# Performance work log

Measured on AMD Instinct MI355X. Metric: run time of the kernel, lower is better.

## Reference

```python
import jax, jax.numpy as jnp
import numpy as np

NF = 64            # nf_effect
N_HISTORY = 3
ADJ_THRESH = 0.12  # float adj_thresh passed to construct_edges
PSTEP = 3


def _relu(x):
    return jnp.maximum(x, 0)


def construct_edges(states, thresh, mask, tool_mask, topk):
    """JAX port of construct_edges_from_states_batch (connect_tools_all=False).
    Returns fixed-shape Rr, Rs of shape (B, N*topk, N); each receiver i owns
    slots [i*topk, (i+1)*topk). Invalid slots are all-zero rows, which is
    math-equivalent to torch's compacted n_rel under all bmms.
    """
    B, N, _ = states.shape
    dt = states.dtype
    d = states[:, :, None, :] - states[:, None, :, :]          # (B,N,N,3)
    dis = jnp.sum(d * d, axis=-1)                              # (B,N,N)
    big = jnp.asarray(1e10, dt)
    m12 = mask[:, :, None] & mask[:, None, :]                  # valid pair
    t12 = tool_mask[:, :, None] & tool_mask[:, None, :]        # tool-tool: cut
    dis = jnp.where(m12 & ~t12, dis, big)
    adj = dis < (thresh * thresh)                              # (B,N,N) bool
    # connect_tools_all=False branch: zero tool-receiver / obj-sender edges
    adj = adj & ~(tool_mask[:, :, None] & mask[:, None, :])
    _, idx = jax.lax.top_k(-dis, topk)                         # (B,N,topk) smallest dis
    valid = jnp.take_along_axis(adj, idx, axis=-1).astype(dt)  # (B,N,topk)
    recv_oh = jnp.eye(N, dtype=dt)                             # (N,N)
    Rr = (valid[..., None] * recv_oh[None, :, None, :]).reshape(B, N * topk, N)
    Rs = (valid[..., None] * jax.nn.one_hot(idx, N, dtype=dt)).reshape(B, N * topk, N)
    return Rr, Rs


def _prop_forward(states, a_cur, s_delta, Rr, Rs,
                  pe_w1, pe_b1, pe_w2, pe_b2,
                  re_w1, re_b1, re_w2, re_b2, re_w3, re_b3,
                  rp_w, rp_b, pp_w, pp_b,
                  pr_w1, pr_b1, pr_w2, pr_b2):
    # s_delta: (B, 3*n_history, N) -> (B, N, 3*n_history)
    s_delta_flat = jnp.transpose(s_delta, (0, 2, 1))
    nh = N_HISTORY
    # relation features: receiver/sender attrs + position difference
    a_r = jnp.einsum('brn,bn->br', Rr, a_cur)[..., None]       # (B,R,1)
    a_s = jnp.einsum('brn,bn->br', Rs, a_cur)[..., None]
    s_r = jnp.einsum('brn,bnd->brd', Rr, states)               # (B,R,3)
    s_s = jnp.einsum('brn,bnd->brd', Rs, states)
    rel_in = jnp.concatenate([a_r, a_s, s_r - s_s], axis=-1)   # (B,R,5)
    # relation encoder: 3-layer MLP, ReLU after each
    h = _relu(rel_in @ re_w1 + re_b1)
    h = _relu(h @ re_w2 + re_b2)
    rel_enc = _relu(h @ re_w3 + re_b3)                         # (B,R,NF)
    # particle encoder: [s_delta history | attrs tiled n_history] -> 12 dims
    p_in = jnp.concatenate(
        [s_delta_flat, jnp.repeat(a_cur[..., None], nh, axis=-1)], axis=-1)
    p_enc = _relu(_relu(p_in @ pe_w1 + pe_b1) @ pe_w2 + pe_b2)  # (B,N,NF)
    effect = p_enc
    for _ in range(PSTEP):
        eff_r = jnp.einsum('brn,bnd->brd', Rr, effect)
        eff_s = jnp.einsum('brn,bnd->brd', Rs, effect)
        rel_eff = _relu(
            jnp.concatenate([rel_enc, eff_r, eff_s], axis=-1) @ rp_w + rp_b)
        agg = jnp.einsum('brn,brd->bnd', Rr, rel_eff)          # Rr^T bmm
        effect = _relu(
            jnp.concatenate([p_enc, agg], axis=-1) @ pp_w + pp_b + effect)
    pred = _relu(effect @ pr_w1 + pr_b1) @ pr_w2 + pr_b2       # (B,N,3)
    return states + pred  # add_delta=True


def setup_inputs():
    key = jax.random.key(0)
    ks = jax.random.split(key, 16)
    B, N = 2, 2048
    states = jax.random.uniform(ks[0], (B, N, 3), dtype=jnp.float32)
    a_cur = jax.random.uniform(ks[1], (B, N), dtype=jnp.float32)
    s_delta = jax.random.normal(ks[2], (B, 3 * N_HISTORY, N), dtype=jnp.float32) * 0.01
    mask = jnp.ones((B, N), dtype=bool)
    tool_mask = jnp.broadcast_to(jnp.arange(N) < N // 20, (B, N))
    s = lambda fan: 1.0 / np.sqrt(fan)
    p = lambda k, sh: jax.random.normal(k, sh, dtype=jnp.float32) * s(sh[0])
    z = lambda n: jnp.zeros((n,), dtype=jnp.float32)
    params = {
        'pe_w1': p(ks[3], (4 * N_HISTORY, NF)), 'pe_b1': z(NF),
        'pe_w2': p(ks[4], (NF, NF)), 'pe_b2': z(NF),
        're_w1': p(ks[5], (5, NF)), 're_b1': z(NF),
        're_w2': p(ks[6], (NF, NF)), 're_b2': z(NF),
        're_w3': p(ks[7], (NF, NF)), 're_b3': z(NF),
        'rp_w': p(ks[8], (3 * NF, NF)), 'rp_b': z(NF),
        'pp_w': p(ks[9], (2 * NF, NF)), 'pp_b': z(NF),
        'pr_w1': p(ks[10], (NF, NF)), 'pr_b1': z(NF),
        'pr_w2': p(ks[11], (NF, 3)), 'pr_b2': z(3),
    }
    return {'states': states, 'a_cur': a_cur, 's_delta': s_delta,
            'mask': mask, 'tool_mask': tool_mask, 'topk': 8, **params}


def reference(states, a_cur, s_delta, mask, tool_mask, topk,
              pe_w1, pe_b1, pe_w2, pe_b2,
              re_w1, re_b1, re_w2, re_b2, re_w3, re_b3,
              rp_w, rp_b, pp_w, pp_b,
              pr_w1, pr_b1, pr_w2, pr_b2):
    Rr, Rs = construct_edges(states, ADJ_THRESH, mask, tool_mask, topk)
    return _prop_forward(states, a_cur, s_delta, Rr, Rs,
                         pe_w1, pe_b1, pe_w2, pe_b2,
                         re_w1, re_b1, re_w2, re_b2, re_w3, re_b3,
                         rp_w, rp_b, pp_w, pp_b,
                         pr_w1, pr_b1, pr_w2, pr_b2)
```

## Files before the change

### kernel.cpp

```cpp
#include <hip/hip_runtime.h>
#include <math.h>

#define DEV __device__ __forceinline__

constexpr int BB = 2, N = 2048, KK = 8;
constexpr int NODES = BB * N;
constexpr int NSLOTS = NODES * KK;
constexpr int NPB = 8;
constexpr int TPB = 512;
constexpr int NBLK = NODES / NPB;

typedef __attribute__((ext_vector_type(8))) short short8v;
typedef __attribute__((ext_vector_type(4))) float float4v;
union S8 { short8v v; unsigned u[4]; unsigned short s[8]; };

DEV int bool_mode(const void* p) {
  unsigned v = *(const unsigned*)p;
  if (v == 0x3f800000u) return 2;
  if (v <= 1u) return 1;
  return 0;
}
DEV bool read_mask(const void* p, int i, int mode) {
  if (mode == 2) return ((const float*)p)[i] != 0.f;
  if (mode == 1) return ((const int*)p)[i] != 0;
  return ((const unsigned char*)p)[i] != 0;
}

DEV unsigned short f2bf(float x) {
  unsigned u = __builtin_bit_cast(unsigned, x);
  return (unsigned short)((u + 0x7FFFu + ((u >> 16) & 1u)) >> 16);
}
DEV unsigned pk2(float a, float b) {
  return (unsigned)f2bf(a) | ((unsigned)f2bf(b) << 16);
}

DEV short8v rdA(const unsigned short* T, int row, int kk0) {
  return *(const short8v*)&T[row * 64 + (kk0 ^ ((row & 7) << 3))];
}
DEV void stage_wT(const float* __restrict__ W, unsigned short* wt, int t) {
  const int f = t & 63, k0 = (t >> 6) * 8;
  S8 p;
  #pragma unroll
  for (int q = 0; q < 4; ++q)
    p.u[q] = pk2(W[(k0 + 2 * q) * 64 + f], W[(k0 + 2 * q + 1) * 64 + f]);
  *(short8v*)&wt[f * 64 + (k0 ^ ((f & 7) << 3))] = p.v;
}
DEV void stage_row8(unsigned short* T, int row, int kq, const float* __restrict__ g) {
  const int k0 = kq * 8;
  float4 v0 = ((const float4*)(g + k0))[0];
  float4 v1 = ((const float4*)(g + k0))[1];
  S8 p;
  p.u[0] = pk2(v0.x, v0.y); p.u[1] = pk2(v0.z, v0.w);
  p.u[2] = pk2(v1.x, v1.y); p.u[3] = pk2(v1.z, v1.w);
  *(short8v*)&T[row * 64 + (k0 ^ ((row & 7) << 3))] = p.v;
}

#define LESS(da, ja, db, jb) ((da) < (db) || ((da) == (db) && (ja) < (jb)))
#define CE(a, b)                                                              \
  {                                                                           \
    bool sw_ = LESS(nd[b], nj[b], nd[a], nj[a]);                              \
    float t_ = nd[a]; int u_ = nj[a];                                         \
    if (sw_) { nd[a] = nd[b]; nj[a] = nj[b]; nd[b] = t_; nj[b] = u_; }        \
  }

struct SEdge { float px[N], py[N], pz[N], padd[N]; };
struct SMlpF { unsigned short A0[4096]; unsigned short A1[4096]; float hb[64 * 9]; };
union SUF { SEdge e; SMlpF m; };

__global__ __launch_bounds__(TPB, 4) void k_front(
    const float* __restrict__ states, const void* maskp, const void* toolp,
    const float* __restrict__ a_cur, const float* __restrict__ s_delta,
    const float* __restrict__ pe_w1, const float* __restrict__ pe_b1,
    const float* __restrict__ pe_w2, const float* __restrict__ pe_b2,
    const float* __restrict__ re_w1, const float* __restrict__ re_b1,
    const float* __restrict__ re_w2, const float* __restrict__ re_b2,
    const float* __restrict__ re_w3, const float* __restrict__ re_b3,
    const float* __restrict__ rp_w, const float* __restrict__ rp_b,
    const float* __restrict__ pp_w, const float* __restrict__ pp_b,
    int* __restrict__ eidx, float* __restrict__ evalid,
    float* __restrict__ p_const, float* __restrict__ rel_const,
    float* __restrict__ eff0) {
  __shared__ SUF su;
  __shared__ unsigned short wt3[3][4096];
  __shared__ int   sl_idx[64];
  __shared__ float sl_val[64];
  const int tid = threadIdx.x;
  const int wav = tid >> 6, lane = tid & 63;
  const int blk = blockIdx.x;
  const int node0 = blk * NPB;
  const int slot0 = blk * 64;
  const int b = node0 >> 11;
  const int mm = bool_mode(maskp), mt = bool_mode(toolp);

  stage_wT(re_w2, wt3[0], tid);
  stage_wT(re_w3, wt3[1], tid);
  stage_wT(rp_w,  wt3[2], tid);

  {
    for (int j = tid; j < N; j += TPB) {
      const float* s = states + (size_t)(b * N + j) * 3;
      su.e.px[j] = s[0]; su.e.py[j] = s[1]; su.e.pz[j] = s[2];
      su.e.padd[j] = read_mask(maskp, b * N + j, mm) ? 0.f : 1e10f;
    }
    __syncthreads();
    const int node = node0 + wav;
    const int i = node & (N - 1);
    const bool mi = read_mask(maskp, node, mm);
    const bool ti = read_mask(toolp, node, mt);
    float td[KK]; int tj[KK];
    #pragma unroll
    for (int k = 0; k < KK; ++k) { td[k] = 3.0e38f; tj[k] = 0; }
    if (mi && !ti) {
      const float sx = su.e.px[i], sy = su.e.py[i], sz = su.e.pz[i];
      #pragma unroll 4
      for (int it = 0; it < N / 64; ++it) {
        int j = lane + it * 64;
        float dx = sx - su.e.px[j], dy = sy - su.e.py[j], dz = sz - su.e.pz[j];
        float dis = __fadd_rn(__fadd_rn(__fmul_rn(dx, dx), __fmul_rn(dy, dy)),
                              __fmul_rn(dz, dz));
        float dd = __fadd_rn(dis, su.e.padd[j]);
        if (dd < td[KK - 1]) {
          float cd = dd; int cj = j;
          #pragma unroll
          for (int m = 0; m < KK; ++m) {
            bool sw = cd < td[m];
            float od = td[m]; int oj = tj[m];
            td[m] = sw ? cd : od; tj[m] = sw ? cj : oj;
            cd = sw ? od : cd;   cj = sw ? oj : cj;
          }
        }
      }
      #pragma unroll
      for (int m = 1; m < 64; m <<= 1) {
        float pd[KK]; int pj[KK];
        #pragma unroll
        for (int r = 0; r < KK; ++r) {
          pd[r] = __shfl_xor(td[r], m);
          pj[r] = __shfl_xor(tj[r], m);
        }
        float nd[KK]; int nj[KK];
        #pragma unroll
        for (int r = 0; r < KK; ++r) {
          float ad = td[r]; int aj = tj[r];
          float bd = pd[KK - 1 - r]; int bj = pj[KK - 1 - r];
          bool tb = LESS(bd, bj, ad, aj);
          nd[r] = tb ? bd : ad; nj[r] = tb ? bj : aj;
        }
        CE(0, 4) CE(1, 5) CE(2, 6) CE(3, 7)
        CE(0, 2) CE(1, 3) CE(4, 6) CE(5, 7)
        CE(0, 1) CE(2, 3) CE(4, 5) CE(6, 7)
        #pragma unroll
        for (int r = 0; r < KK; ++r) { td[r] = nd[r]; tj[r] = nj[r]; }
      }
    }
    if (lane == 0) {
      const float T2 = (float)(0.12 * 0.12);
      const bool ok = mi && !ti;
      #pragma unroll
      for (int k = 0; k < KK; ++k) {
        float v = (ok && td[k] < T2) ? 1.f : 0.f;
        sl_idx[wav * KK + k] = tj[k];
        sl_val[wav * KK + k] = v;
        eidx[(node0 + wav) * KK + k] = tj[k];
        evalid[(node0 + wav) * KK + k] = v;
      }
    }
    __syncthreads();
  }

  {
    float* hb = su.m.hb;
    const int nd = node0 + wav;
    const int i = nd & (N - 1);
    const int f = lane;
    float sd[9];
    #pragma unroll
    for (int k = 0; k < 9; ++k) sd[k] = s_delta[(b * 9 + k) * N + i];
    const float a = a_cur[nd];
    float x = pe_b1[f];
    #pragma unroll
    for (int k = 0; k < 9; ++k) x = fmaf(sd[k], pe_w1[k * 64 + f], x);
    x = fmaf(a, pe_w1[576 + f] + pe_w1[640 + f] + pe_w1[704 + f], x);
    x = fmaxf(x, 0.f);
    hb[f * 9 + wav] = x;
    __syncthreads();
    float y = pe_b2[f];
    #pragma unroll 4
    for (int k = 0; k < 64; ++k) y = fmaf(hb[k * 9 + wav], pe_w2[k * 64 + f], y);
    y = fmaxf(y, 0.f);
    eff0[(size_t)nd * 64 + f] = y;
    __syncthreads();
    hb[f * 9 + wav] = y;
    __syncthreads();
    float z = pp_b[f];
    #pragma unroll 4
    for (int k = 0; k < 64; ++k) z = fmaf(hb[k * 9 + wav], pp_w[k * 64 + f], z);
    p_const[(size_t)nd * 64 + f] = z;
    __syncthreads();
  }

  {
    unsigned short* A0 = su.m.A0;
    unsigned short* A1 = su.m.A1;
    const int f0 = __builtin_amdgcn_readfirstlane(wav * 8);
    const int col = lane;
    const int nd = node0 + (col >> 3);
    const int nb = nd & ~(N - 1);
    const int j = nb + sl_idx[col];
    const float a_r = a_cur[nd], a_s = a_cur[j];
    const float dx = states[nd * 3]     - states[j * 3];
    const float dy = states[nd * 3 + 1] - states[j * 3 + 1];
    const float dz = states[nd * 3 + 2] - states[j * 3 + 2];
    float t[8];
    #pragma unroll
    for (int u = 0; u < 8; ++u) {
      const int f = f0 + u;
      float x = re_b1[f];
      x = fmaf(a_r, re_w1[f], x);
      x = fmaf(a_s, re_w1[64 + f], x);
      x = fmaf(dx, re_w1[128 + f], x);
      x = fmaf(dy, re_w1[192 + f], x);
      x = fmaf(dz, re_w1[256 + f], x);
      t[u] = fmaxf(x, 0.f);
    }
    #pragma unroll
    for (int u = 0; u < 8; u += 2) {
      int idx = col * 64 + ((f0 + u) ^ ((col & 7) << 3));
      *(unsigned*)&A0[idx] = pk2(t[u], t[u + 1]);
    }
    __syncthreads();

    const int m = wav & 3, h = wav >> 2;
    const int n0t = 2 * h, n1t = n0t + 1;
    const int rowA = m * 16 + (lane & 15);
    const int fc0 = n0t * 16 + (lane & 15), fc1 = n1t * 16 + (lane & 15);
    const unsigned long long vm = __ballot(sl_val[lane] != 0.f);

    {
      float b0 = re_b2[fc0], b1 = re_b2[fc1];
      float4v c0 = {b0, b0, b0, b0}, c1 = {b1, b1, b1, b1};
      #pragma unroll
      for (int ks = 0; ks < 2; ++ks) {
        const int kk0 = ks * 32 + (lane >> 4) * 8;
        short8v a  = rdA(A0, rowA, kk0);
        short8v w0 = rdA(wt3[0], fc0, kk0);
        short8v w1 = rdA(wt3[0], fc1, kk0);
        c0 = __builtin_amdgcn_mfma_f32_16x16x32_bf16(a, w0, c0, 0, 0, 0);
        c1 = __builtin_amdgcn_mfma_f32_16x16x32_bf16(a, w1, c1, 0, 0, 0);
      }
      #pragma unroll
      for (int r = 0; r < 4; ++r) {
        int slot = m * 16 + (lane >> 4) * 4 + r;
        A1[slot * 64 + (fc0 ^ ((slot & 7) << 3))] = f2bf(fmaxf(c0[r], 0.f));
        A1[slot * 64 + (fc1 ^ ((slot & 7) << 3))] = f2bf(fmaxf(c1[r], 0.f));
      }
    }
    __syncthreads();
    {
      float b0 = re_b3[fc0], b1 = re_b3[fc1];
      float4v c0 = {b0, b0, b0, b0}, c1 = {b1, b1, b1, b1};
      #pragma unroll
      for (int ks = 0; ks < 2; ++ks) {
        const int kk0 = ks * 32 + (lane >> 4) * 8;
        short8v a  = rdA(A1, rowA, kk0);
        short8v w0 = rdA(wt3[1], fc0, kk0);
        short8v w1 = rdA(wt3[1], fc1, kk0);
        c0 = __builtin_amdgcn_mfma_f32_16x16x32_bf16(a, w0, c0, 0, 0, 0);
        c1 = __builtin_amdgcn_mfma_f32_16x16x32_bf16(a, w1, c1, 0, 0, 0);
      }
      #pragma unroll
      for (int r = 0; r < 4; ++r) {
        int slot = m * 16 + (lane >> 4) * 4 + r;
        A0[slot * 64 + (fc0 ^ ((slot & 7) << 3))] = f2bf(fmaxf(c0[r], 0.f));
        A0[slot * 64 + (fc1 ^ ((slot & 7) << 3))] = f2bf(fmaxf(c1[r], 0.f));
      }
    }
    __syncthreads();
    {
      float b0 = rp_b[fc0], b1 = rp_b[fc1];
      float4v c0 = {b0, b0, b0, b0}, c1 = {b1, b1, b1, b1};
      #pragma unroll
      for (int ks = 0; ks < 2; ++ks) {
        const int kk0 = ks * 32 + (lane >> 4) * 8;
        short8v a  = rdA(A0, rowA, kk0);
        short8v w0 = rdA(wt3[2], fc0, kk0);
        short8v w1 = rdA(wt3[2], fc1, kk0);
        c0 = __builtin_amdgcn_mfma_f32_16x16x32_bf16(a, w0, c0, 0, 0, 0);
        c1 = __builtin_amdgcn_mfma_f32_16x16x32_bf16(a, w1, c1, 0, 0, 0);
      }
      #pragma unroll
      for (int r = 0; r < 4; ++r) {
        int slot = m * 16 + (lane >> 4) * 4 + r;
        float v = (float)((vm >> slot) & 1ull);
        rel_const[(size_t)(slot0 + slot) * 64 + fc0] = c0[r] * v;
        rel_const[(size_t)(slot0 + slot) * 64 + fc1] = c1[r] * v;
      }
    }
  }
}

template <int HEAD>
__global__ __launch_bounds__(TPB, 4) void k_prop(
    const float* __restrict__ rp_w, const float* __restrict__ pp_w,
    const int* __restrict__ eidx, const float* __restrict__ evalid,
    const float* __restrict__ p_const, const float* __restrict__ rel_const,
    const float* __restrict__ effIn, float* __restrict__ effOut,
    const float* __restrict__ states,
    const float* __restrict__ pr_w1, const float* __restrict__ pr_b1,
    const float* __restrict__ pr_w2, const float* __restrict__ pr_b2,
    float* __restrict__ out) {
  __shared__ unsigned short AS[4096];
  __shared__ unsigned short EN[512];
  __shared__ unsigned short wt2[2][4096];
  __shared__ float agg[8 * 64];
  const int tid = threadIdx.x;
  const int wav = tid >> 6, lane = tid & 63;
  const int blk = blockIdx.x;
  const int node0 = blk * NPB;
  const int slot0 = blk * 64;
  const int nb = node0 & ~(N - 1);

  stage_wT(rp_w + 4096, wt2[0], tid);
  stage_wT(rp_w + 8192, wt2[1], tid);
  {
    const int slot = tid >> 3, kq = tid & 7;
    const int j = nb + eidx[slot0 + slot];
    stage_row8(AS, slot, kq, effIn + (size_t)j * 64);
  }
  if (tid < 64) {
    const int n = tid >> 3, kq = tid & 7;
    stage_row8(EN, n, kq, effIn + (size_t)(node0 + n) * 64);
  }
  const unsigned long long vm = __ballot(evalid[slot0 + lane] != 0.f);
  __syncthreads();

  {
    const int m = wav & 3, h = wav >> 2;
    const int n0t = 2 * h, n1t = n0t + 1;
    const int rowA = m * 16 + (lane & 15);
    const int nodeR = rowA >> 3;
    const int fc0 = n0t * 16 + (lane & 15), fc1 = n1t * 16 + (lane & 15);
    float4v c0, c1;
    #pragma unroll
    for (int r = 0; r < 4; ++r) {
      int slot = m * 16 + (lane >> 4) * 4 + r;
      c0[r] = rel_const[(size_t)(slot0 + slot) * 64 + fc0];
      c1[r] = rel_const[(size_t)(slot0 + slot) * 64 + fc1];
    }
    #pragma unroll
    for (int ks = 0; ks < 2; ++ks) {
      const int kk0 = ks * 32 + (lane >> 4) * 8;
      short8v aR = rdA(EN, nodeR, kk0);
      short8v aS = rdA(AS, rowA, kk0);
      short8v w10 = rdA(wt2[0], fc0, kk0);
      short8v w11 = rdA(wt2[0], fc1, kk0);
      short8v w20 = rdA(wt2[1], fc0, kk0);
      short8v w21 = rdA(wt2[1], fc1, kk0);
      c0 = __builtin_amdgcn_mfma_f32_16x16x32_bf16(aR, w10, c0, 0, 0, 0);
      c1 = __builtin_amdgcn_mfma_f32_16x16x32_bf16(aR, w11, c1, 0, 0, 0);
      c0 = __builtin_amdgcn_mfma_f32_16x16x32_bf16(aS, w20, c0, 0, 0, 0);
      c1 = __builtin_amdgcn_mfma_f32_16x16x32_bf16(aS, w21, c1, 0, 0, 0);
    }
    float s0 = 0.f, s1 = 0.f;
    #pragma unroll
    for (int r = 0; r < 4; ++r) {
      int slot = m * 16 + (lane >> 4) * 4 + r;
      float v = (float)((vm >> slot) & 1ull);
      s0 += fmaxf(c0[r], 0.f) * v;
      s1 += fmaxf(c1[r], 0.f) * v;
    }
    s0 += __shfl_xor(s0, 16);
    s1 += __shfl_xor(s1, 16);
    if (((lane >> 4) & 1) == 0) {
      const int an = m * 2 + (lane >> 5);
      agg[an * 64 + fc0] = s0;
      agg[an * 64 + fc1] = s1;
    }
  }
  __syncthreads();

  const int onode = node0 + wav;
  float o = p_const[(size_t)onode * 64 + lane];
  #pragma unroll 4
  for (int g = 0; g < 64; ++g)
    o = fmaf(agg[wav * 64 + g], pp_w[4096 + g * 64 + lane], o);
  const float er = effIn[(size_t)onode * 64 + lane];
  const float ov = fmaxf(o + er, 0.f);
  if (HEAD == 0) {
    effOut[(size_t)onode * 64 + lane] = ov;
  } else {
    __syncthreads();
    agg[wav * 64 + lane] = ov;
    __syncthreads();
    float hh = pr_b1[lane];
    #pragma unroll 4
    for (int k = 0; k < 64; ++k)
      hh = fmaf(agg[wav * 64 + k], pr_w1[k * 64 + lane], hh);
    hh = fmaxf(hh, 0.f);
    float p0 = hh * pr_w2[lane * 3];
    float p1 = hh * pr_w2[lane * 3 + 1];
    float p2 = hh * pr_w2[lane * 3 + 2];
    #pragma unroll
    for (int m = 1; m < 64; m <<= 1) {
      p0 += __shfl_xor(p0, m);
      p1 += __shfl_xor(p1, m);
      p2 += __shfl_xor(p2, m);
    }
    if (lane == 0) {
      out[onode * 3]     = states[onode * 3]     + p0 + pr_b2[0];
      out[onode * 3 + 1] = states[onode * 3 + 1] + p1 + pr_b2[1];
      out[onode * 3 + 2] = states[onode * 3 + 2] + p2 + pr_b2[2];
    }
  }
}

extern "C" void kernel_launch(void* const* d_in, const int* in_sizes, int n_in,
                              void* d_out, int out_size, void* d_ws, size_t ws_size,
                              hipStream_t stream) {
  const float* states  = (const float*)d_in[0];
  const float* a_cur   = (const float*)d_in[1];
  const float* s_delta = (const float*)d_in[2];
  const void*  maskp   = d_in[3];
  const void*  toolp   = d_in[4];
  const float* pe_w1 = (const float*)d_in[6];
  const float* pe_b1 = (const float*)d_in[7];
  const float* pe_w2 = (const float*)d_in[8];
  const float* pe_b2 = (const float*)d_in[9];
  const float* re_w1 = (const float*)d_in[10];
  const float* re_b1 = (const float*)d_in[11];
  const float* re_w2 = (const float*)d_in[12];
  const float* re_b2 = (const float*)d_in[13];
  const float* re_w3 = (const float*)d_in[14];
  const float* re_b3 = (const float*)d_in[15];
  const float* rp_w  = (const float*)d_in[16];
  const float* rp_b  = (const float*)d_in[17];
  const float* pp_w  = (const float*)d_in[18];
  const float* pp_b  = (const float*)d_in[19];
  const float* pr_w1 = (const float*)d_in[20];
  const float* pr_b1 = (const float*)d_in[21];
  const float* pr_w2 = (const float*)d_in[22];
  const float* pr_b2 = (const float*)d_in[23];

  char* w = (char*)d_ws;
  int*   eidx      = (int*)w;   w += (size_t)NSLOTS * 4;
  float* evalid    = (float*)w; w += (size_t)NSLOTS * 4;
  float* p_const   = (float*)w; w += (size_t)NODES * 64 * 4;
  float* rel_const = (float*)w; w += (size_t)NSLOTS * 64 * 4;
  float* effA      = (float*)w; w += (size_t)NODES * 64 * 4;
  float* effB      = (float*)w; w += (size_t)NODES * 64 * 4;
  float* out       = (float*)d_out;

  k_front<<<NBLK, TPB, 0, stream>>>(states, maskp, toolp, a_cur, s_delta,
      pe_w1, pe_b1, pe_w2, pe_b2, re_w1, re_b1, re_w2, re_b2, re_w3, re_b3,
      rp_w, rp_b, pp_w, pp_b, eidx, evalid, p_const, rel_const, effA);
  k_prop<0><<<NBLK, TPB, 0, stream>>>(rp_w, pp_w, eidx, evalid, p_const,
      rel_const, effA, effB, states, pr_w1, pr_b1, pr_w2, pr_b2, out);
  k_prop<0><<<NBLK, TPB, 0, stream>>>(rp_w, pp_w, eidx, evalid, p_const,
      rel_const, effB, effA, states, pr_w1, pr_b1, pr_w2, pr_b2, out);
  k_prop<1><<<NBLK, TPB, 0, stream>>>(rp_w, pp_w, eidx, evalid, p_const,
      rel_const, effA, effB, states, pr_w1, pr_b1, pr_w2, pr_b2, out);
}
```

Baseline: 161.8 us.

## Fuse front and propagation kernels into one persistent kernel with grid barriers

Merges the edge-construction/encoder kernel and the three propagation kernels into a single launch, with software grid barriers (atomic counter plus spin) between propagation steps. Per-block state such as edge indices, validity, p_const, relation constants and the node's own effect is kept in registers and LDS instead of going through global memory. This removes three kernel launches and the related global traffic. In exchange it depends on all 512 blocks being co-resident, which needs 2 blocks per CU on 256 CUs, adds a memset and spin-wait overhead, and raises LDS use per block.

```diff
diff --git a/kernel.cpp b/kernel.cpp
--- a/kernel.cpp
+++ b/kernel.cpp
@@ -5,7 +5,6 @@
 
 constexpr int BB = 2, N = 2048, KK = 8;
 constexpr int NODES = BB * N;
-constexpr int NSLOTS = NODES * KK;
 constexpr int NPB = 8;
 constexpr int TPB = 512;
 constexpr int NBLK = NODES / NPB;
@@ -64,10 +63,21 @@
   }
 
 struct SEdge { float px[N], py[N], pz[N], padd[N]; };
-struct SMlpF { unsigned short A0[4096]; unsigned short A1[4096]; float hb[64 * 9]; };
-union SUF { SEdge e; SMlpF m; };
-
-__global__ __launch_bounds__(TPB, 4) void k_front(
+
+DEV void gbar(unsigned* bar, int idx) {
+  __syncthreads();
+  if (threadIdx.x == 0) {
+    __threadfence();
+    __hip_atomic_fetch_add(&bar[idx], 1u, __ATOMIC_RELEASE, __HIP_MEMORY_SCOPE_AGENT);
+    while (__hip_atomic_load(&bar[idx], __ATOMIC_ACQUIRE,
+                             __HIP_MEMORY_SCOPE_AGENT) < (unsigned)NBLK)
+      __builtin_amdgcn_s_sleep(2);
+    __threadfence();
+  }
+  __syncthreads();
+}
+
+__global__ __launch_bounds__(TPB, 4) void k_all(
     const float* __restrict__ states, const void* maskp, const void* toolp,
     const float* __restrict__ a_cur, const float* __restrict__ s_delta,
     const float* __restrict__ pe_w1, const float* __restrict__ pe_b1,
@@ -77,30 +87,32 @@
     const float* __restrict__ re_w3, const float* __restrict__ re_b3,
     const float* __restrict__ rp_w, const float* __restrict__ rp_b,
     const float* __restrict__ pp_w, const float* __restrict__ pp_b,
-    int* __restrict__ eidx, float* __restrict__ evalid,
-    float* __restrict__ p_const, float* __restrict__ rel_const,
-    float* __restrict__ eff0) {
-  __shared__ SUF su;
-  __shared__ unsigned short wt3[3][4096];
+    const float* __restrict__ pr_w1, const float* __restrict__ pr_b1,
+    const float* __restrict__ pr_w2, const float* __restrict__ pr_b2,
+    float* __restrict__ effA, float* __restrict__ effB,
+    unsigned* __restrict__ bar, float* __restrict__ out) {
+  __shared__ unsigned short wt_rp0[4096], wt_rp1[4096], wt_rp2[4096];
+  __shared__ char Ubuf[32768];
   __shared__ int   sl_idx[64];
   __shared__ float sl_val[64];
   const int tid = threadIdx.x;
   const int wav = tid >> 6, lane = tid & 63;
   const int blk = blockIdx.x;
   const int node0 = blk * NPB;
-  const int slot0 = blk * 64;
   const int b = node0 >> 11;
+  const int nb = node0 & ~(N - 1);
   const int mm = bool_mode(maskp), mt = bool_mode(toolp);
 
-  stage_wT(re_w2, wt3[0], tid);
-  stage_wT(re_w3, wt3[1], tid);
-  stage_wT(rp_w,  wt3[2], tid);
+  stage_wT(rp_w,        wt_rp0, tid);
+  stage_wT(rp_w + 4096, wt_rp1, tid);
+  stage_wT(rp_w + 8192, wt_rp2, tid);
 
   {
+    SEdge* se = (SEdge*)Ubuf;
     for (int j = tid; j < N; j += TPB) {
       const float* s = states + (size_t)(b * N + j) * 3;
-      su.e.px[j] = s[0]; su.e.py[j] = s[1]; su.e.pz[j] = s[2];
-      su.e.padd[j] = read_mask(maskp, b * N + j, mm) ? 0.f : 1e10f;
+      se->px[j] = s[0]; se->py[j] = s[1]; se->pz[j] = s[2];
+      se->padd[j] = read_mask(maskp, b * N + j, mm) ? 0.f : 1e10f;
     }
     __syncthreads();
     const int node = node0 + wav;
@@ -111,14 +123,14 @@
     #pragma unroll
     for (int k = 0; k < KK; ++k) { td[k] = 3.0e38f; tj[k] = 0; }
     if (mi && !ti) {
-      const float sx = su.e.px[i], sy = su.e.py[i], sz = su.e.pz[i];
+      const float sx = se->px[i], sy = se->py[i], sz = se->pz[i];
       #pragma unroll 4
       for (int it = 0; it < N / 64; ++it) {
         int j = lane + it * 64;
-        float dx = sx - su.e.px[j], dy = sy - su.e.py[j], dz = sz - su.e.pz[j];
+        float dx = sx - se->px[j], dy = sy - se->py[j], dz = sz - se->pz[j];
         float dis = __fadd_rn(__fadd_rn(__fmul_rn(dx, dx), __fmul_rn(dy, dy)),
                               __fmul_rn(dz, dz));
-        float dd = __fadd_rn(dis, su.e.padd[j]);
+        float dd = __fadd_rn(dis, se->padd[j]);
         if (dd < td[KK - 1]) {
           float cd = dd; int cj = j;
           #pragma unroll
@@ -158,18 +170,20 @@
       const bool ok = mi && !ti;
       #pragma unroll
       for (int k = 0; k < KK; ++k) {
-        float v = (ok && td[k] < T2) ? 1.f : 0.f;
         sl_idx[wav * KK + k] = tj[k];
-        sl_val[wav * KK + k] = v;
-        eidx[(node0 + wav) * KK + k] = tj[k];
-        evalid[(node0 + wav) * KK + k] = v;
-      }
-    }
-    __syncthreads();
-  }
-
+        sl_val[wav * KK + k] = (ok && td[k] < T2) ? 1.f : 0.f;
+      }
+    }
+    __syncthreads();
+  }
+
+  float pc, ev;
   {
-    float* hb = su.m.hb;
+    unsigned short* wt_enc0 = (unsigned short*)(Ubuf + 16384);
+    unsigned short* wt_enc1 = (unsigned short*)(Ubuf + 24576);
+    stage_wT(re_w2, wt_enc0, tid);
+    stage_wT(re_w3, wt_enc1, tid);
+    float* hb = (float*)Ubuf;
     const int nd = node0 + wav;
     const int i = nd & (N - 1);
     const int f = lane;
@@ -188,24 +202,27 @@
     #pragma unroll 4
     for (int k = 0; k < 64; ++k) y = fmaf(hb[k * 9 + wav], pe_w2[k * 64 + f], y);
     y = fmaxf(y, 0.f);
-    eff0[(size_t)nd * 64 + f] = y;
+    effA[(size_t)nd * 64 + f] = y;
+    ev = y;
     __syncthreads();
     hb[f * 9 + wav] = y;
     __syncthreads();
     float z = pp_b[f];
     #pragma unroll 4
     for (int k = 0; k < 64; ++k) z = fmaf(hb[k * 9 + wav], pp_w[k * 64 + f], z);
-    p_const[(size_t)nd * 64 + f] = z;
+    pc = z;
     __syncthreads();
   }
 
   {
-    unsigned short* A0 = su.m.A0;
-    unsigned short* A1 = su.m.A1;
+    unsigned short* A0 = (unsigned short*)Ubuf;
+    unsigned short* A1 = (unsigned short*)(Ubuf + 8192);
+    unsigned short* wt_enc0 = (unsigned short*)(Ubuf + 16384);
+    unsigned short* wt_enc1 = (unsigned short*)(Ubuf + 24576);
+    float* relC = (float*)(Ubuf + 16384);
     const int f0 = __builtin_amdgcn_readfirstlane(wav * 8);
     const int col = lane;
     const int nd = node0 + (col >> 3);
-    const int nb = nd & ~(N - 1);
     const int j = nb + sl_idx[col];
     const float a_r = a_cur[nd], a_s = a_cur[j];
     const float dx = states[nd * 3]     - states[j * 3];
@@ -229,13 +246,10 @@
       *(unsigned*)&A0[idx] = pk2(t[u], t[u + 1]);
     }
     __syncthreads();
-
     const int m = wav & 3, h = wav >> 2;
-    const int n0t = 2 * h, n1t = n0t + 1;
     const int rowA = m * 16 + (lane & 15);
-    const int fc0 = n0t * 16 + (lane & 15), fc1 = n1t * 16 + (lane & 15);
+    const int fc0 = (2 * h) * 16 + (lane & 15), fc1 = fc0 + 16;
     const unsigned long long vm = __ballot(sl_val[lane] != 0.f);
-
     {
       float b0 = re_b2[fc0], b1 = re_b2[fc1];
       float4v c0 = {b0, b0, b0, b0}, c1 = {b1, b1, b1, b1};
@@ -243,8 +257,8 @@
       for (int ks = 0; ks < 2; ++ks) {
         const int kk0 = ks * 32 + (lane >> 4) * 8;
         short8v a  = rdA(A0, rowA, kk0);
-        short8v w0 = rdA(wt3[0], fc0, kk0);
-        short8v w1 = rdA(wt3[0], fc1, kk0);
+        short8v w0 = rdA(wt_enc0, fc0, kk0);
+        short8v w1 = rdA(wt_enc0, fc1, kk0);
         c0 = __builtin_amdgcn_mfma_f32_16x16x32_bf16(a, w0, c0, 0, 0, 0);
         c1 = __builtin_amdgcn_mfma_f32_16x16x32_bf16(a, w1, c1, 0, 0, 0);
       }
@@ -263,8 +277,8 @@
       for (int ks = 0; ks < 2; ++ks) {
         const int kk0 = ks * 32 + (lane >> 4) * 8;
         short8v a  = rdA(A1, rowA, kk0);
-        short8v w0 = rdA(wt3[1], fc0, kk0);
-        short8v w1 = rdA(wt3[1], fc1, kk0);
+        short8v w0 = rdA(wt_enc1, fc0, kk0);
+        short8v w1 = rdA(wt_enc1, fc1, kk0);
         c0 = __builtin_amdgcn_mfma_f32_16x16x32_bf16(a, w0, c0, 0, 0, 0);
         c1 = __builtin_amdgcn_mfma_f32_16x16x32_bf16(a, w1, c1, 0, 0, 0);
       }
@@ -283,8 +297,8 @@
       for (int ks = 0; ks < 2; ++ks) {
         const int kk0 = ks * 32 + (lane >> 4) * 8;
         short8v a  = rdA(A0, rowA, kk0);
-        short8v w0 = rdA(wt3[2], fc0, kk0);
-        short8v w1 = rdA(wt3[2], fc1, kk0);
+        short8v w0 = rdA(wt_rp0, fc0, kk0);
+        short8v w1 = rdA(wt_rp0, fc1, kk0);
         c0 = __builtin_amdgcn_mfma_f32_16x16x32_bf16(a, w0, c0, 0, 0, 0);
         c1 = __builtin_amdgcn_mfma_f32_16x16x32_bf16(a, w1, c1, 0, 0, 0);
       }
@@ -292,105 +306,89 @@
       for (int r = 0; r < 4; ++r) {
         int slot = m * 16 + (lane >> 4) * 4 + r;
         float v = (float)((vm >> slot) & 1ull);
-        rel_const[(size_t)(slot0 + slot) * 64 + fc0] = c0[r] * v;
-        rel_const[(size_t)(slot0 + slot) * 64 + fc1] = c1[r] * v;
-      }
-    }
-  }
-}
-
-template <int HEAD>
-__global__ __launch_bounds__(TPB, 4) void k_prop(
-    const float* __restrict__ rp_w, const float* __restrict__ pp_w,
-    const int* __restrict__ eidx, const float* __restrict__ evalid,
-    const float* __restrict__ p_const, const float* __restrict__ rel_const,
-    const float* __restrict__ effIn, float* __restrict__ effOut,
-    const float* __restrict__ states,
-    const float* __restrict__ pr_w1, const float* __restrict__ pr_b1,
-    const float* __restrict__ pr_w2, const float* __restrict__ pr_b2,
-    float* __restrict__ out) {
-  __shared__ unsigned short AS[4096];
-  __shared__ unsigned short EN[512];
-  __shared__ unsigned short wt2[2][4096];
-  __shared__ float agg[8 * 64];
-  const int tid = threadIdx.x;
-  const int wav = tid >> 6, lane = tid & 63;
-  const int blk = blockIdx.x;
-  const int node0 = blk * NPB;
-  const int slot0 = blk * 64;
-  const int nb = node0 & ~(N - 1);
-
-  stage_wT(rp_w + 4096, wt2[0], tid);
-  stage_wT(rp_w + 8192, wt2[1], tid);
+        relC[slot * 64 + fc0] = c0[r] * v;
+        relC[slot * 64 + fc1] = c1[r] * v;
+      }
+    }
+  }
+
+  gbar(bar, 0);
+
+  auto prop = [&](const float* __restrict__ effIn, float* __restrict__ effOut) {
+    unsigned short* AS = (unsigned short*)Ubuf;
+    unsigned short* EN = (unsigned short*)(Ubuf + 8192);
+    float* agg = (float*)(Ubuf + 9216);
+    float* relC = (float*)(Ubuf + 16384);
+    {
+      const int slot = tid >> 3, kq = tid & 7;
+      const int j = nb + sl_idx[slot];
+      stage_row8(AS, slot, kq, effIn + (size_t)j * 64);
+    }
+    EN[wav * 64 + (lane ^ ((wav & 7) << 3))] = f2bf(ev);
+    const unsigned long long vm = __ballot(sl_val[lane] != 0.f);
+    __syncthreads();
+    {
+      const int m = wav & 3, h = wav >> 2;
+      const int rowA = m * 16 + (lane & 15);
+      const int nodeR = rowA >> 3;
+      const int fc0 = (2 * h) * 16 + (lane & 15), fc1 = fc0 + 16;
+      float4v c0, c1;
+      #pragma unroll
+      for (int r = 0; r < 4; ++r) {
+        int slot = m * 16 + (lane >> 4) * 4 + r;
+        c0[r] = relC[slot * 64 + fc0];
+        c1[r] = relC[slot * 64 + fc1];
+      }
+      #pragma unroll
+      for (int ks = 0; ks < 2; ++ks) {
+        const int kk0 = ks * 32 + (lane >> 4) * 8;
+        short8v aR = rdA(EN, nodeR, kk0);
+        short8v aS = rdA(AS, rowA, kk0);
+        short8v w10 = rdA(wt_rp1, fc0, kk0);
+        short8v w11 = rdA(wt_rp1, fc1, kk0);
+        short8v w20 = rdA(wt_rp2, fc0, kk0);
+        short8v w21 = rdA(wt_rp2, fc1, kk0);
+        c0 = __builtin_amdgcn_mfma_f32_16x16x32_bf16(aR, w10, c0, 0, 0, 0);
+        c1 = __builtin_amdgcn_mfma_f32_16x16x32_bf16(aR, w11, c1, 0, 0, 0);
+        c0 = __builtin_amdgcn_mfma_f32_16x16x32_bf16(aS, w20, c0, 0, 0, 0);
+        c1 = __builtin_amdgcn_mfma_f32_16x16x32_bf16(aS, w21, c1, 0, 0, 0);
+      }
+      float s0 = 0.f, s1 = 0.f;
+      #pragma unroll
+      for (int r = 0; r < 4; ++r) {
+        int slot = m * 16 + (lane >> 4) * 4 + r;
+        float v = (float)((vm >> slot) & 1ull);
+        s0 += fmaxf(c0[r], 0.f) * v;
+        s1 += fmaxf(c1[r], 0.f) * v;
+      }
+      s0 += __shfl_xor(s0, 16);
+      s1 += __shfl_xor(s1, 16);
+      if (((lane >> 4) & 1) == 0) {
+        const int an = m * 2 + (lane >> 5);
+        agg[an * 64 + fc0] = s0;
+        agg[an * 64 + fc1] = s1;
+      }
+    }
+    __syncthreads();
+    float o = pc;
+    #pragma unroll 4
+    for (int g = 0; g < 64; ++g)
+      o = fmaf(agg[wav * 64 + g], pp_w[4096 + g * 64 + lane], o);
+    float ov = fmaxf(o + ev, 0.f);
+    if (effOut) effOut[(size_t)(node0 + wav) * 64 + lane] = ov;
+    ev = ov;
+    __syncthreads();
+  };
+
+  prop(effA, effB);
+  gbar(bar, 1);
+  prop(effB, effA);
+  gbar(bar, 2);
+  prop(effA, nullptr);
+
   {
-    const int slot = tid >> 3, kq = tid & 7;
-    const int j = nb + eidx[slot0 + slot];
-    stage_row8(AS, slot, kq, effIn + (size_t)j * 64);
-  }
-  if (tid < 64) {
-    const int n = tid >> 3, kq = tid & 7;
-    stage_row8(EN, n, kq, effIn + (size_t)(node0 + n) * 64);
-  }
-  const unsigned long long vm = __ballot(evalid[slot0 + lane] != 0.f);
-  __syncthreads();
-
-  {
-    const int m = wav & 3, h = wav >> 2;
-    const int n0t = 2 * h, n1t = n0t + 1;
-    const int rowA = m * 16 + (lane & 15);
-    const int nodeR = rowA >> 3;
-    const int fc0 = n0t * 16 + (lane & 15), fc1 = n1t * 16 + (lane & 15);
-    float4v c0, c1;
-    #pragma unroll
-    for (int r = 0; r < 4; ++r) {
-      int slot = m * 16 + (lane >> 4) * 4 + r;
-      c0[r] = rel_const[(size_t)(slot0 + slot) * 64 + fc0];
-      c1[r] = rel_const[(size_t)(slot0 + slot) * 64 + fc1];
-    }
-    #pragma unroll
-    for (int ks = 0; ks < 2; ++ks) {
-      const int kk0 = ks * 32 + (lane >> 4) * 8;
-      short8v aR = rdA(EN, nodeR, kk0);
-      short8v aS = rdA(AS, rowA, kk0);
-      short8v w10 = rdA(wt2[0], fc0, kk0);
-      short8v w11 = rdA(wt2[0], fc1, kk0);
-      short8v w20 = rdA(wt2[1], fc0, kk0);
-      short8v w21 = rdA(wt2[1], fc1, kk0);
-      c0 = __builtin_amdgcn_mfma_f32_16x16x32_bf16(aR, w10, c0, 0, 0, 0);
-      c1 = __builtin_amdgcn_mfma_f32_16x16x32_bf16(aR, w11, c1, 0, 0, 0);
-      c0 = __builtin_amdgcn_mfma_f32_16x16x32_bf16(aS, w20, c0, 0, 0, 0);
-      c1 = __builtin_amdgcn_mfma_f32_16x16x32_bf16(aS, w21, c1, 0, 0, 0);
-    }
-    float s0 = 0.f, s1 = 0.f;
-    #pragma unroll
-    for (int r = 0; r < 4; ++r) {
-      int slot = m * 16 + (lane >> 4) * 4 + r;
-      float v = (float)((vm >> slot) & 1ull);
-      s0 += fmaxf(c0[r], 0.f) * v;
-      s1 += fmaxf(c1[r], 0.f) * v;
-    }
-    s0 += __shfl_xor(s0, 16);
-    s1 += __shfl_xor(s1, 16);
-    if (((lane >> 4) & 1) == 0) {
-      const int an = m * 2 + (lane >> 5);
-      agg[an * 64 + fc0] = s0;
-      agg[an * 64 + fc1] = s1;
-    }
-  }
-  __syncthreads();
-
-  const int onode = node0 + wav;
-  float o = p_const[(size_t)onode * 64 + lane];
-  #pragma unroll 4
-  for (int g = 0; g < 64; ++g)
-    o = fmaf(agg[wav * 64 + g], pp_w[4096 + g * 64 + lane], o);
-  const float er = effIn[(size_t)onode * 64 + lane];
-  const float ov = fmaxf(o + er, 0.f);
-  if (HEAD == 0) {
-    effOut[(size_t)onode * 64 + lane] = ov;
-  } else {
-    __syncthreads();
-    agg[wav * 64 + lane] = ov;
+    float* agg = (float*)(Ubuf + 9216);
+    agg[wav * 64 + lane] = ev;
     __syncthreads();
     float hh = pr_b1[lane];
     #pragma unroll 4
@@ -407,6 +405,7 @@
       p2 += __shfl_xor(p2, m);
     }
     if (lane == 0) {
+      const int onode = node0 + wav;
       out[onode * 3]     = states[onode * 3]     + p0 + pr_b2[0];
       out[onode * 3 + 1] = states[onode * 3 + 1] + p1 + pr_b2[1];
       out[onode * 3 + 2] = states[onode * 3 + 2] + p2 + pr_b2[2];
@@ -442,21 +441,13 @@
   const float* pr_b2 = (const float*)d_in[23];
 
   char* w = (char*)d_ws;
-  int*   eidx      = (int*)w;   w += (size_t)NSLOTS * 4;
-  float* evalid    = (float*)w; w += (size_t)NSLOTS * 4;
-  float* p_const   = (float*)w; w += (size_t)NODES * 64 * 4;
-  float* rel_const = (float*)w; w += (size_t)NSLOTS * 64 * 4;
-  float* effA      = (float*)w; w += (size_t)NODES * 64 * 4;
-  float* effB      = (float*)w; w += (size_t)NODES * 64 * 4;
-  float* out       = (float*)d_out;
-
-  k_front<<<NBLK, TPB, 0, stream>>>(states, maskp, toolp, a_cur, s_delta,
+  float* effA = (float*)w; w += (size_t)NODES * 64 * 4;
+  float* effB = (float*)w; w += (size_t)NODES * 64 * 4;
+  unsigned* bar = (unsigned*)w;
+
+  hipMemsetAsync(bar, 0, 4 * sizeof(unsigned), stream);
+  k_all<<<NBLK, TPB, 0, stream>>>(states, maskp, toolp, a_cur, s_delta,
       pe_w1, pe_b1, pe_w2, pe_b2, re_w1, re_b1, re_w2, re_b2, re_w3, re_b3,
-      rp_w, rp_b, pp_w, pp_b, eidx, evalid, p_const, rel_const, effA);
-  k_prop<0><<<NBLK, TPB, 0, stream>>>(rp_w, pp_w, eidx, evalid, p_const,
-      rel_const, effA, effB, states, pr_w1, pr_b1, pr_w2, pr_b2, out);
-  k_prop<0><<<NBLK, TPB, 0, stream>>>(rp_w, pp_w, eidx, evalid, p_const,
-      rel_const, effB, effA, states, pr_w1, pr_b1, pr_w2, pr_b2, out);
-  k_prop<1><<<NBLK, TPB, 0, stream>>>(rp_w, pp_w, eidx, evalid, p_const,
-      rel_const, effA, effB, states, pr_w1, pr_b1, pr_w2, pr_b2, out);
-}
+      rp_w, rp_b, pp_w, pp_b, pr_w1, pr_b1, pr_w2, pr_b2,
+      effA, effB, bar, (float*)d_out);
+}
```

After: 417.6 us. 158% more time.
